# Optimization experiments

Measured on AMD Instinct MI355X. Metric: run time of the kernel, lower is better.

Reference implementation:

```python
import jax, jax.numpy as jnp
import numpy as np

NUM_LAYERS = 6
DIM = 512
VOCAB = 50257
HEADS = 8
EXPERTS = 8
TOPK = 2
LN_EPS = 1e-5


def setup_inputs() -> dict:
    key = jax.random.key(0)
    ks = jax.random.split(key, 9)
    d, L, E = DIM, NUM_LAYERS, EXPERTS
    return {
        'input_ids': jax.random.randint(ks[0], (2, 1024), 0, VOCAB),
        'embed': jax.random.normal(ks[1], (VOCAB, d), dtype=jnp.float32) * 0.02,
        'qkv_w': jax.random.normal(ks[2], (L, 3 * d, d), dtype=jnp.float32) * 0.02,
        'out_w': jax.random.normal(ks[3], (L, d, d), dtype=jnp.float32) * 0.02,
        'router_w': jax.random.normal(ks[4], (L, E, d), dtype=jnp.float32) * 0.02,
        'router_b': jnp.zeros((L, E), dtype=jnp.float32),
        'w1': jax.random.normal(ks[5], (L, E, 2 * d, d), dtype=jnp.float32) * 0.02,
        'b1': jnp.zeros((L, E, 2 * d), dtype=jnp.float32),
        'w2': jax.random.normal(ks[6], (L, E, d, 2 * d), dtype=jnp.float32) * 0.02,
        'b2': jnp.zeros((L, E, d), dtype=jnp.float32),
        'ln_g': jnp.ones((L, d), dtype=jnp.float32),
        'ln_b': jnp.zeros((L, d), dtype=jnp.float32),
        'head_w': jax.random.normal(ks[7], (VOCAB, d), dtype=jnp.float32) * 0.02,
    }


def _bit_weight(w):
    # BitNet 1.58b training-mode effective weight (STE forward value):
    # scale = mean|w| per output row; w_eff = round(w/scale).clip(-1,1) * scale
    scale = jnp.clip(jnp.mean(jnp.abs(w), axis=-1, keepdims=True), 1e-5, None)
    wq = jnp.clip(jnp.round(w / scale), -1.0, 1.0)
    w_ste = jax.lax.stop_gradient(wq - w) + w
    return w_ste * scale


def _layer_norm(x, g, b):
    mu = jnp.mean(x, axis=-1, keepdims=True)
    var = jnp.mean(jnp.square(x - mu), axis=-1, keepdims=True)
    return (x - mu) * jax.lax.rsqrt(var + LN_EPS) * g + b


def _attention(x, qkv_w, out_w):
    B, Lq, D = x.shape
    hd = D // HEADS
    qkv = (x @ qkv_w.T).reshape(B, Lq, 3, HEADS, hd).transpose(2, 0, 3, 1, 4)
    q, k, v = qkv[0], qkv[1], qkv[2]  # [B,H,L,hd]
    attn = jax.nn.softmax(jnp.einsum('bhqd,bhkd->bhqk', q, k) * hd ** -0.5, axis=-1)
    o = jnp.einsum('bhqk,bhkd->bhqd', attn, v).transpose(0, 2, 1, 3).reshape(B, Lq, D)
    return o @ out_w.T


def _moe(x, rw, rb, w1, b1, w2, b2, g, beta):
    B, Lq, D = x.shape
    N = B * Lq
    xf = x.reshape(N, D)
    probs = jax.nn.softmax(xf @ rw.T + rb, axis=-1)  # [N,E]
    vals, idx = jax.lax.top_k(probs, TOPK)
    vals = vals / (jnp.sum(vals, axis=-1, keepdims=True) + 1e-8)
    # combine weights: [N,E] (top-k indices are distinct, so sum == scatter)
    cw = jnp.sum(jax.nn.one_hot(idx, EXPERTS, dtype=xf.dtype) * vals[..., None], axis=1)
    we1 = _bit_weight(w1)  # [E,2D,D]
    we2 = _bit_weight(w2)  # [E,D,2D]
    h = jax.nn.gelu(jnp.einsum('nd,efd->enf', xf, we1) + b1[:, None, :], approximate=False)
    y = jnp.einsum('enf,edf->end', h, we2) + b2[:, None, :]  # [E,N,D]
    out = jnp.einsum('ne,end->nd', cw, y)
    return _layer_norm(out + xf, g, beta).reshape(B, Lq, D)


def reference(input_ids, embed, qkv_w, out_w, router_w, router_b, w1, b1, w2, b2, ln_g, ln_b, head_w):
    x = embed[input_ids]  # [B,L,D]
    for l in range(NUM_LAYERS):
        x = x + _attention(x, qkv_w[l], out_w[l])
        x = _moe(x, router_w[l], router_b[l], w1[l], b1[l], w2[l], b2[l], ln_g[l], ln_b[l])
    return x @ head_w.T  # logits [B,L,V]
```

## Files before the change

kernel.cpp:

```cpp
#include <hip/hip_runtime.h>
#include <math.h>
#include <stdint.h>

#define NLAYER 6
#define DIMD 512
#define HEADS 8
#define HD 64
#define EXPERTS 8
#define SEQ 1024
#define NTOK 2048
#define FF 1024
#define VOCABN 50257
#define HROWS 50304

typedef __bf16 bf16;
typedef __bf16 bf16x8 __attribute__((ext_vector_type(8)));
typedef __bf16 bf16x4 __attribute__((ext_vector_type(4)));
typedef float f32x4 __attribute__((ext_vector_type(4)));

__device__ __forceinline__ void gl_lds16(const void* g, void* l) {
  __builtin_amdgcn_global_load_lds(
      (const __attribute__((address_space(1))) void*)(uintptr_t)g,
      (__attribute__((address_space(3))) void*)(uintptr_t)l, 16, 0, 0);
}

#define LDSW(row, kg) (((row) * 32) + ((((kg) ^ (((row) >> 1) & 3))) << 3))

template <int BNT>
__global__ __launch_bounds__(256) void k_mfma_gemm(
    const bf16* __restrict__ A0, const bf16* __restrict__ A1,
    const bf16* __restrict__ B0, const bf16* __restrict__ B1,
    float* __restrict__ Cf, bf16* __restrict__ Cb0, bf16* __restrict__ Cb1,
    bf16* __restrict__ Cb2, bf16* __restrict__ E0, bf16* __restrict__ E1,
    bf16* __restrict__ E2, int M, int N, int K,
    long sA, long sB, long sCf, long sCb,
    const float* __restrict__ colScale, int csStride,
    const float* __restrict__ bias, int biasStride,
    const float* __restrict__ residual, int act, int mode,
    const int* __restrict__ mLimit, const int* __restrict__ aperm,
    int outmode) {
  constexpr int NI = BNT / 32;
  __shared__ __align__(16) bf16 As[128 * 32];
  __shared__ __align__(16) bf16 Bs[BNT * 32];
  int tid = threadIdx.x;
  int z = blockIdx.z;
  int nwg = gridDim.x * gridDim.y;
  int flat = blockIdx.y * gridDim.x + blockIdx.x;
  int qq = nwg >> 3, rr = nwg & 7;
  int xcd = flat & 7, ii = flat >> 3;
  int swz = (xcd < rr ? xcd * (qq + 1) : rr * (qq + 1) + (xcd - rr) * qq) + ii;
  int m0 = (swz % gridDim.x) * 128, n0 = (swz / gridDim.x) * BNT;
  if (mLimit && m0 >= mLimit[z]) return;
  int w = tid >> 6, lane = tid & 63;
  int wm = (w >> 1) * 64, wn = (w & 1) * (16 * NI);
  int r15 = lane & 15, kg = lane >> 4;

  int pa[3] = {0, 0, 0}, pb[3] = {0, 0, 0};
  int np = 1;
  if (mode == 3) {
    np = 2; pa[1] = 1;
  } else if (mode == 5) {
    np = 3;
    pa[1] = 0; pb[1] = 1; pa[2] = 1; pb[2] = 0;
  }

  f32x4 acc[4][NI] = {};
  int srow = tid >> 2;
  int scol = (((tid & 3) ^ ((tid >> 3) & 3))) << 3;
  long arow0, arow1;
  if (aperm) {
    arow0 = aperm[z * 2048 + m0 + srow];
    arow1 = aperm[z * 2048 + m0 + 64 + srow];
  } else {
    arow0 = m0 + srow;
    arow1 = m0 + 64 + srow;
  }
  const bf16* PA[2] = {A0, A1};
  const bf16* PB[2] = {B0, B1};
  bf16* la0 = &As[tid * 8];
  bf16* la1 = &As[64 * 32 + tid * 8];
  bf16* lb0 = &Bs[tid * 8];

  for (int p = 0; p < np; ++p) {
    const bf16* Az = PA[pa[p]] + (long)z * sA;
    const bf16* Bz = PB[pb[p]] + (long)z * sB;
    const bf16* ga0 = Az + arow0 * K + scol;
    const bf16* ga1 = Az + arow1 * K + scol;
    const bf16* gb0 = Bz + (long)(n0 + srow) * K + scol;
    const bf16* gb1 = (BNT == 128) ? Bz + (long)(n0 + 64 + srow) * K + scol
                                   : nullptr;
    for (int k0 = 0; k0 < K; k0 += 32) {
      gl_lds16(ga0, la0);
      gl_lds16(ga1, la1);
      gl_lds16(gb0, lb0);
      if constexpr (BNT == 128) gl_lds16(gb1, &Bs[64 * 32 + tid * 8]);
      ga0 += 32; ga1 += 32; gb0 += 32;
      if constexpr (BNT == 128) gb1 += 32;
      __syncthreads();
      bf16x8 af[4], bfr[NI];
#pragma unroll
      for (int mi = 0; mi < 4; ++mi) {
        int rowA = wm + mi * 16 + r15;
        af[mi] = *(const bf16x8*)&As[LDSW(rowA, kg)];
      }
#pragma unroll
      for (int ni = 0; ni < NI; ++ni) {
        int rowB = wn + ni * 16 + r15;
        bfr[ni] = *(const bf16x8*)&Bs[LDSW(rowB, kg)];
      }
#pragma unroll
      for (int mi = 0; mi < 4; ++mi)
#pragma unroll
        for (int ni = 0; ni < NI; ++ni)
          acc[mi][ni] = __builtin_amdgcn_mfma_f32_16x16x32_bf16(
              af[mi], bfr[ni], acc[mi][ni], 0, 0, 0);
      __syncthreads();
    }
  }

#pragma unroll
  for (int mi = 0; mi < 4; ++mi) {
    int rbase = m0 + wm + mi * 16 + kg * 4;
#pragma unroll
    for (int ni = 0; ni < NI; ++ni) {
      int col = n0 + wn + ni * 16 + r15;
      if (col >= N) continue;
      float scl = colScale ? colScale[z * csStride + col] : 1.f;
      float bv = bias ? bias[z * biasStride + col] : 0.f;
#pragma unroll
      for (int reg = 0; reg < 4; ++reg) {
        int row = rbase + reg;
        float v = acc[mi][ni][reg] * scl + bv;
        if (act) v = 0.5f * v * (1.f + erff(v * 0.70710678118654752f));
        if (residual) v += residual[(long)row * N + col];
        if (outmode == 2) {
          int b = row >> 10, qt = row & 1023;
          if (n0 < 512) {
            float qv = v * 0.125f;
            int h = col >> 6, d = col & 63;
            long dst = ((long)(b * 8 + h)) * ((long)SEQ * HD) +
                       (long)qt * HD + d;
            bf16 h0 = (bf16)qv;
            Cb0[dst] = h0;
            Cb1[dst] = (bf16)(qv - (float)h0);
          } else if (n0 < 1024) {
            int c2 = col - 512;
            int h = c2 >> 6, d = c2 & 63;
            long dst = ((long)(b * 8 + h)) * ((long)SEQ * HD) +
                       (long)qt * HD + d;
            bf16 h0 = (bf16)v;
            Cb2[dst] = h0;
            E0[dst] = (bf16)(v - (float)h0);
          } else {
            int c2 = col - 1024;
            int h = c2 >> 6, d = c2 & 63;
            long dst = ((long)(b * 8 + h)) * ((long)HD * SEQ) +
                       (long)d * SEQ + qt;
            bf16 h0 = (bf16)v;
            E1[dst] = h0;
            E2[dst] = (bf16)(v - (float)h0);
          }
          continue;
        }
        if (Cf) Cf[z * sCf + (long)row * N + col] = v;
        if (Cb0) {
          long cib = z * sCb + (long)row * N + col;
          bf16 h0 = (bf16)v;
          Cb0[cib] = h0;
          if (Cb1) {
            float r = v - (float)h0;
            Cb1[cib] = (bf16)r;
          }
        }
      }
    }
  }
}

__global__ __launch_bounds__(256) void k_fattn(
    const bf16* __restrict__ q0b, const bf16* __restrict__ q1b,
    const bf16* __restrict__ k0b, const bf16* __restrict__ k1b,
    const bf16* __restrict__ vt0, const bf16* __restrict__ vt1,
    bf16* __restrict__ at0, bf16* __restrict__ at1) {
  __shared__ __align__(16) bf16 Ks[2][128 * 64];
  __shared__ __align__(16) bf16 Vs[2][64 * 128];
  __shared__ __align__(16) bf16 Ps[2][64 * 128];
  int tid = threadIdx.x;
  int bh = blockIdx.y;
  int q0 = blockIdx.x * 64;
  int w = tid >> 6, lane = tid & 63;
  int r15 = lane & 15, kg = lane >> 4;
  const long bhQK = (long)bh * SEQ * HD;
  const long bhV = (long)bh * HD * SEQ;

  bf16x8 qa0[2], qa1[2];
  {
    long qoff = bhQK + (long)(q0 + w * 16 + r15) * HD;
#pragma unroll
    for (int ks = 0; ks < 2; ++ks) {
      qa0[ks] = *(const bf16x8*)&q0b[qoff + ks * 32 + kg * 8];
      qa1[ks] = *(const bf16x8*)&q1b[qoff + ks * 32 + kg * 8];
    }
  }

  auto stageK = [&](int kt) {
#pragma unroll
    for (int i = 0; i < 4; ++i) {
      int L = tid + i * 256;
      int row = L >> 3, pc = L & 7;
      int gc = pc ^ (row & 7);
      long gsrc = bhQK + (long)(kt * 128 + row) * HD + gc * 8;
      gl_lds16(k0b + gsrc, &Ks[0][L * 8]);
      gl_lds16(k1b + gsrc, &Ks[1][L * 8]);
    }
  };
  auto stageV = [&](int kt) {
#pragma unroll
    for (int i = 0; i < 4; ++i) {
      int L = tid + i * 256;
      int row = L >> 4, pc = L & 15;
      int gc = pc ^ (row & 15);
      long gsrc = bhV + (long)row * SEQ + kt * 128 + gc * 8;
      gl_lds16(vt0 + gsrc, &Vs[0][L * 8]);
      gl_lds16(vt1 + gsrc, &Vs[1][L * 8]);
    }
  };
  auto computeS = [&](f32x4* sf) {
#pragma unroll
    for (int kc = 0; kc < 8; ++kc) {
      f32x4 a = {};
      int rowB = kc * 16 + r15;
#pragma unroll
      for (int ks = 0; ks < 2; ++ks) {
        int pc = (ks * 4 + kg) ^ (rowB & 7);
        bf16x8 b0 = *(const bf16x8*)&Ks[0][rowB * 64 + pc * 8];
        bf16x8 b1 = *(const bf16x8*)&Ks[1][rowB * 64 + pc * 8];
        a = __builtin_amdgcn_mfma_f32_16x16x32_bf16(qa0[ks], b0, a, 0, 0, 0);
        a = __builtin_amdgcn_mfma_f32_16x16x32_bf16(qa0[ks], b1, a, 0, 0, 0);
        a = __builtin_amdgcn_mfma_f32_16x16x32_bf16(qa1[ks], b0, a, 0, 0, 0);
      }
      sf[kc] = a;
    }
  };

  float m[4], l[4];
#pragma unroll
  for (int r = 0; r < 4; ++r) { m[r] = -1e30f; l[r] = 0.f; }

  for (int kt = 0; kt < SEQ / 128; ++kt) {
    stageK(kt);
    __syncthreads();
    f32x4 sf[8];
    computeS(sf);
#pragma unroll
    for (int r = 0; r < 4; ++r) {
      float tm = sf[0][r];
#pragma unroll
      for (int kc = 1; kc < 8; ++kc) tm = fmaxf(tm, sf[kc][r]);
      tm = fmaxf(tm, __shfl_xor(tm, 1));
      tm = fmaxf(tm, __shfl_xor(tm, 2));
      tm = fmaxf(tm, __shfl_xor(tm, 4));
      tm = fmaxf(tm, __shfl_xor(tm, 8));
      float mn = fmaxf(m[r], tm);
      float corr = __expf(m[r] - mn);
      float s = 0.f;
#pragma unroll
      for (int kc = 0; kc < 8; ++kc) s += __expf(sf[kc][r] - mn);
      s += __shfl_xor(s, 1);
      s += __shfl_xor(s, 2);
      s += __shfl_xor(s, 4);
      s += __shfl_xor(s, 8);
      l[r] = l[r] * corr + s;
      m[r] = mn;
    }
    __syncthreads();
  }

  float invl[4];
#pragma unroll
  for (int r = 0; r < 4; ++r) invl[r] = 1.f / l[r];

  f32x4 oacc[4] = {};
  for (int kt = 0; kt < SEQ / 128; ++kt) {
    stageK(kt);
    stageV(kt);
    __syncthreads();
    f32x4 sf[8];
    computeS(sf);
#pragma unroll
    for (int kc = 0; kc < 8; ++kc) {
#pragma unroll
      for (int r = 0; r < 4; ++r) {
        float p = __expf(sf[kc][r] - m[r]) * invl[r];
        bf16 h0 = (bf16)p;
        bf16 h1 = (bf16)(p - (float)h0);
        int qrow = w * 16 + kg * 4 + r;
        int kcol = kc * 16 + r15;
        int pc = (kcol >> 3) ^ (qrow & 15);
        int addr = qrow * 128 + pc * 8 + (kcol & 7);
        Ps[0][addr] = h0;
        Ps[1][addr] = h1;
      }
    }
    __syncthreads();
    bf16x8 pa0[4], pa1[4];
    int rowP = w * 16 + r15;
#pragma unroll
    for (int ks = 0; ks < 4; ++ks) {
      int pc = (ks * 4 + kg) ^ (rowP & 15);
      pa0[ks] = *(const bf16x8*)&Ps[0][rowP * 128 + pc * 8];
      pa1[ks] = *(const bf16x8*)&Ps[1][rowP * 128 + pc * 8];
    }
#pragma unroll
    for (int dg = 0; dg < 4; ++dg) {
      int rowV = dg * 16 + r15;
#pragma unroll
      for (int ks = 0; ks < 4; ++ks) {
        int pc = (ks * 4 + kg) ^ (rowV & 15);
        bf16x8 v0 = *(const bf16x8*)&Vs[0][rowV * 128 + pc * 8];
        bf16x8 v1 = *(const bf16x8*)&Vs[1][rowV * 128 + pc * 8];
        oacc[dg] = __builtin_amdgcn_mfma_f32_16x16x32_bf16(pa0[ks], v0,
                                                           oacc[dg], 0, 0, 0);
        oacc[dg] = __builtin_amdgcn_mfma_f32_16x16x32_bf16(pa0[ks], v1,
                                                           oacc[dg], 0, 0, 0);
        oacc[dg] = __builtin_amdgcn_mfma_f32_16x16x32_bf16(pa1[ks], v0,
                                                           oacc[dg], 0, 0, 0);
      }
    }
    __syncthreads();
  }

  int b = bh >> 3, h = bh & 7;
#pragma unroll
  for (int dg = 0; dg < 4; ++dg) {
#pragma unroll
    for (int r = 0; r < 4; ++r) {
      int qrow = q0 + w * 16 + kg * 4 + r;
      int d = dg * 16 + r15;
      long dst = ((long)(b * SEQ + qrow)) * DIMD + h * HD + d;
      float v = oacc[dg][r];
      bf16 h0 = (bf16)v;
      at0[dst] = h0;
      at1[dst] = (bf16)(v - (float)h0);
    }
  }
}

__global__ __launch_bounds__(256) void k_hgemm(const bf16* __restrict__ A,
                                               const bf16* __restrict__ Bt,
                                               float* __restrict__ C,
                                               int M, int N, int K) {
  __shared__ __align__(16) bf16 As[128 * 64];
  __shared__ __align__(16) bf16 Bs[128 * 64];
  int tid = threadIdx.x;
  int nwg = gridDim.x * gridDim.y;
  int flat = blockIdx.y * gridDim.x + blockIdx.x;
  int qq = nwg >> 3, rr = nwg & 7;
  int xcd = flat & 7, ii = flat >> 3;
  int swz = (xcd < rr ? xcd * (qq + 1) : rr * (qq + 1) + (xcd - rr) * qq) + ii;
  int m0 = (swz % gridDim.x) * 128, n0 = (swz / gridDim.x) * 128;
  int w = tid >> 6, lane = tid & 63;
  int wm = (w >> 1) * 64, wn = (w & 1) * 64;
  int r15 = lane & 15, kg = lane >> 4;
  int srow = tid >> 3;
  int scol = (((tid & 7) ^ ((tid >> 3) & 7))) << 3;
  const bf16* ga = A + (long)(m0 + srow) * K + scol;
  const bf16* gb = Bt + (long)(n0 + srow) * K + scol;
  f32x4 acc[4][4] = {};
  for (int k0 = 0; k0 < K; k0 += 64) {
#pragma unroll
    for (int i = 0; i < 4; ++i) {
      gl_lds16(ga + (long)i * 32 * K + k0, &As[i * 2048 + tid * 8]);
      gl_lds16(gb + (long)i * 32 * K + k0, &Bs[i * 2048 + tid * 8]);
    }
    __syncthreads();
#pragma unroll
    for (int kk = 0; kk < 2; ++kk) {
      bf16x8 af[4], bf_[4];
#pragma unroll
      for (int mi = 0; mi < 4; ++mi) {
        int rowA = wm + mi * 16 + r15;
        af[mi] = *(const bf16x8*)
            &As[rowA * 64 + ((((kk * 4 + kg) ^ (rowA & 7))) << 3)];
      }
#pragma unroll
      for (int ni = 0; ni < 4; ++ni) {
        int rowB = wn + ni * 16 + r15;
        bf_[ni] = *(const bf16x8*)
            &Bs[rowB * 64 + ((((kk * 4 + kg) ^ (rowB & 7))) << 3)];
      }
#pragma unroll
      for (int mi = 0; mi < 4; ++mi)
#pragma unroll
        for (int ni = 0; ni < 4; ++ni)
          acc[mi][ni] = __builtin_amdgcn_mfma_f32_16x16x32_bf16(
              af[mi], bf_[ni], acc[mi][ni], 0, 0, 0);
    }
    __syncthreads();
  }
#pragma unroll
  for (int mi = 0; mi < 4; ++mi) {
    int rbase = m0 + wm + mi * 16 + kg * 4;
#pragma unroll
    for (int ni = 0; ni < 4; ++ni) {
      int col = n0 + wn + ni * 16 + r15;
      if (col >= N) continue;
#pragma unroll
      for (int reg = 0; reg < 4; ++reg)
        C[(long)(rbase + reg) * N + col] = acc[mi][ni][reg];
    }
  }
}

__global__ __launch_bounds__(256) void k_embed(const int* __restrict__ ids,
                                               const float* __restrict__ E,
                                               float* __restrict__ xf,
                                               bf16* __restrict__ x0,
                                               bf16* __restrict__ x1) {
  int i = blockIdx.x * 256 + threadIdx.x;
  if (i >= NTOK * DIMD) return;
  int n = i >> 9, d = i & 511;
  float v = E[(long)ids[n] * DIMD + d];
  xf[i] = v;
  bf16 b0 = (bf16)v;
  x0[i] = b0;
  x1[i] = (bf16)(v - (float)b0);
}

__global__ __launch_bounds__(256) void k_prepw(const float* __restrict__ qw,
                                               const float* __restrict__ ow,
                                               bf16* __restrict__ qw0,
                                               bf16* __restrict__ qw1,
                                               bf16* __restrict__ ow0,
                                               bf16* __restrict__ ow1) {
  const long n8q = (long)3 * DIMD * DIMD / 8;
  long i = (long)blockIdx.x * 256 + threadIdx.x;
  const float* s;
  bf16 *d0, *d1;
  long j;
  if (i < n8q) {
    s = qw; d0 = qw0; d1 = qw1; j = i;
  } else {
    s = ow; d0 = ow0; d1 = ow1; j = i - n8q;
  }
  const float4* s4 = (const float4*)s;
  float4 a = s4[2 * j], b = s4[2 * j + 1];
  float vv[8] = {a.x, a.y, a.z, a.w, b.x, b.y, b.z, b.w};
  bf16x8 o0, o1;
#pragma unroll
  for (int k = 0; k < 8; ++k) {
    float v = vv[k];
    bf16 h0 = (bf16)v;
    o0[k] = h0;
    o1[k] = (bf16)(v - (float)h0);
  }
  ((bf16x8*)d0)[j] = o0;
  ((bf16x8*)d1)[j] = o1;
}

__global__ __launch_bounds__(256) void k_headconv(const float* __restrict__ s,
                                                  bf16* __restrict__ d) {
  long i = (long)blockIdx.x * 256 + threadIdx.x;
  long n8 = (long)HROWS * DIMD / 8;
  if (i >= n8) return;
  long row = i / (DIMD / 8);
  bf16x8 o;
  if (row < VOCABN) {
    const float4* s4 = (const float4*)s;
    float4 a = s4[2 * i], b = s4[2 * i + 1];
    o[0] = (bf16)a.x; o[1] = (bf16)a.y; o[2] = (bf16)a.z; o[3] = (bf16)a.w;
    o[4] = (bf16)b.x; o[5] = (bf16)b.y; o[6] = (bf16)b.z; o[7] = (bf16)b.w;
  } else {
    o = (bf16x8)(bf16)0.f;
  }
  ((bf16x8*)d)[i] = o;
}

__global__ __launch_bounds__(64) void k_router(const float* __restrict__ x,
                                               const float* __restrict__ rw,
                                               const float* __restrict__ rb,
                                               int* __restrict__ top2,
                                               float* __restrict__ v2) {
  int n = blockIdx.x;
  int t = threadIdx.x;
  int e = t >> 3, part = t & 7;
  __shared__ float red[64];
  const float* xr = x + (long)n * DIMD;
  const float* wr = rw + (long)e * DIMD;
  float d = 0.f;
  int c0 = part * 64;
#pragma unroll
  for (int c = 0; c < 64; c += 4) {
    float4 xv = *(const float4*)(xr + c0 + c);
    float4 wv = *(const float4*)(wr + c0 + c);
    d += xv.x * wv.x + xv.y * wv.y + xv.z * wv.z + xv.w * wv.w;
  }
  red[t] = d;
  __syncthreads();
  if (t < 8) {
    float logit = rb[t];
    for (int pp = 0; pp < 8; ++pp) logit += red[t * 8 + pp];
    red[t] = logit;
  }
  __syncthreads();
  if (t == 0) {
    float p2[8];
    float m = -1e30f;
    for (int i = 0; i < 8; ++i) m = fmaxf(m, red[i]);
    float s = 0.f;
    for (int i = 0; i < 8; ++i) { p2[i] = expf(red[i] - m); s += p2[i]; }
    for (int i = 0; i < 8; ++i) p2[i] /= s;
    int i1 = 0;
    for (int i = 1; i < 8; ++i) if (p2[i] > p2[i1]) i1 = i;
    int i2 = (i1 == 0) ? 1 : 0;
    for (int i = 0; i < 8; ++i) {
      if (i == i1 || i == i2) continue;
      if (p2[i] > p2[i2]) i2 = i;
    }
    float sum = p2[i1] + p2[i2] + 1e-8f;
    top2[2 * n] = i1;
    top2[2 * n + 1] = i2;
    v2[2 * n] = p2[i1] / sum;
    v2[2 * n + 1] = p2[i2] / sum;
  }
}

__global__ __launch_bounds__(256) void k_expcnt(const int* __restrict__ top2,
                                                int* __restrict__ perm,
                                                int* __restrict__ tokpos,
                                                int* __restrict__ cnt,
                                                bf16* __restrict__ zx0,
                                                bf16* __restrict__ zx1) {
  int e = blockIdx.x, t = threadIdx.x;
  if (e == 0) {
    for (int c = t; c < DIMD; c += 256) {
      zx0[c] = (bf16)0.f;
      zx1[c] = (bf16)0.f;
    }
  }
  __shared__ int sc[256];
  int fl[8];
  int f = 0;
#pragma unroll
  for (int j = 0; j < 8; ++j) {
    int n = t * 8 + j;
    int m = (top2[2 * n] == e || top2[2 * n + 1] == e) ? 1 : 0;
    fl[j] = m;
    f += m;
  }
  sc[t] = f;
  __syncthreads();
  for (int o = 1; o < 256; o <<= 1) {
    int v = (t >= o) ? sc[t - o] : 0;
    __syncthreads();
    sc[t] += v;
    __syncthreads();
  }
  int pos = sc[t] - f;
#pragma unroll
  for (int j = 0; j < 8; ++j) {
    if (fl[j]) {
      int n = t * 8 + j;
      perm[e * 2048 + pos] = n;
      int jj = (top2[2 * n] == e) ? 0 : 1;
      tokpos[2 * n + jj] = e * 2048 + pos;
      ++pos;
    }
  }
  int total = sc[255];
  int cpad = (total + 127) & ~127;
  for (int i = total + t; i < cpad; i += 256) perm[e * 2048 + i] = 2048;
  if (t == 0) cnt[e] = total;
}

__global__ __launch_bounds__(256) void k_bitw2(const float* __restrict__ w1l,
                                               const float* __restrict__ w2l,
                                               bf16* __restrict__ we1q,
                                               float* __restrict__ s1,
                                               bf16* __restrict__ we2q,
                                               float* __restrict__ s2) {
  int blk = blockIdx.x;
  int t = threadIdx.x;
  const float* wr;
  bf16* outr;
  float* sOut;
  int cols;
  if (blk < EXPERTS * FF) {
    cols = DIMD;
    wr = w1l + (long)blk * cols;
    outr = we1q + (long)blk * cols;
    sOut = s1 + blk;
  } else {
    int row = blk - EXPERTS * FF;
    cols = FF;
    wr = w2l + (long)row * cols;
    outr = we2q + (long)row * cols;
    sOut = s2 + row;
  }
  float acc = 0.f;
  for (int c = t; c < cols; c += 256) acc += fabsf(wr[c]);
  __shared__ float red[256];
  red[t] = acc;
  __syncthreads();
  for (int off = 128; off; off >>= 1) {
    if (t < off) red[t] += red[t + off];
    __syncthreads();
  }
  float scale = fmaxf(red[0] / (float)cols, 1e-5f);
  if (t == 0) *sOut = scale;
  for (int c = t; c < cols; c += 256) {
    float qv = rintf(wr[c] / scale);
    qv = fmaxf(-1.f, fminf(1.f, qv));
    outr[c] = (bf16)qv;
  }
}

__global__ __launch_bounds__(128) void k_lncomb(
    const float* __restrict__ yg, const int* __restrict__ tokpos,
    const float* __restrict__ v2, const float* __restrict__ xBf,
    const float* __restrict__ g, const float* __restrict__ b,
    float* __restrict__ xof, bf16* __restrict__ x0, bf16* __restrict__ x1) {
  int n = blockIdx.x;
  int t = threadIdx.x;
  __shared__ float red[128];
  long tp0 = tokpos[2 * n], tp1 = tokpos[2 * n + 1];
  float w0 = v2[2 * n], w1 = v2[2 * n + 1];
  const float* y0 = yg + tp0 * DIMD;
  const float* y1 = yg + tp1 * DIMD;
  float u[4];
  float s = 0.f;
#pragma unroll
  for (int i = 0; i < 4; ++i) {
    int d = t + i * 128;
    float v = xBf[(long)n * DIMD + d] + w0 * y0[d] + w1 * y1[d];
    u[i] = v;
    s += v;
  }
  red[t] = s;
  __syncthreads();
  for (int off = 64; off; off >>= 1) {
    if (t < off) red[t] += red[t + off];
    __syncthreads();
  }
  float mu = red[0] / (float)DIMD;
  __syncthreads();
  float var = 0.f;
#pragma unroll
  for (int i = 0; i < 4; ++i) {
    float d = u[i] - mu;
    var += d * d;
  }
  red[t] = var;
  __syncthreads();
  for (int off = 64; off; off >>= 1) {
    if (t < off) red[t] += red[t + off];
    __syncthreads();
  }
  float inv = 1.f / sqrtf(red[0] / (float)DIMD + 1e-5f);
#pragma unroll
  for (int i = 0; i < 4; ++i) {
    int c = t + i * 128;
    float v = (u[i] - mu) * inv * g[c] + b[c];
    long oi = (long)n * DIMD + c;
    xof[oi] = v;
    bf16 b0 = (bf16)v;
    x0[oi] = b0;
    x1[oi] = (bf16)(v - (float)b0);
  }
}

extern "C" void kernel_launch(void* const* d_in, const int* in_sizes, int n_in,
                              void* d_out, int out_size, void* d_ws, size_t ws_size,
                              hipStream_t stream) {
  const int* ids = (const int*)d_in[0];
  const float* embed = (const float*)d_in[1];
  const float* qkv_w = (const float*)d_in[2];
  const float* out_w = (const float*)d_in[3];
  const float* router_w = (const float*)d_in[4];
  const float* router_b = (const float*)d_in[5];
  const float* w1 = (const float*)d_in[6];
  const float* b1 = (const float*)d_in[7];
  const float* w2 = (const float*)d_in[8];
  const float* b2 = (const float*)d_in[9];
  const float* ln_g = (const float*)d_in[10];
  const float* ln_b = (const float*)d_in[11];
  const float* head_w = (const float*)d_in[12];
  float* out = (float*)d_out;

  char* base = (char*)d_ws;
  size_t off = 0;
  auto alloc = [&](size_t bytes) -> void* {
    void* p = base + off;
    off += (bytes + 255) & ~(size_t)255;
    return p;
  };
  const size_t ND = (size_t)NTOK * DIMD;
  float* xAf = (float*)alloc(ND * 4);
  float* xBf = (float*)alloc(ND * 4);
  int* top2 = (int*)alloc((size_t)NTOK * 2 * 4);
  float* v2 = (float*)alloc((size_t)NTOK * 2 * 4);
  int* perm = (int*)alloc((size_t)EXPERTS * 2048 * 4);
  int* tokpos = (int*)alloc((size_t)NTOK * 2 * 4);
  int* cntb = (int*)alloc(64);
  bf16* xA0 = (bf16*)alloc(ND * 2);
  bf16* xA1 = (bf16*)alloc(ND * 2);
  bf16* xB0 = (bf16*)alloc((ND + DIMD) * 2);
  bf16* xB1 = (bf16*)alloc((ND + DIMD) * 2);
  bf16* at0 = (bf16*)alloc(ND * 2);
  bf16* at1 = (bf16*)alloc(ND * 2);
  bf16* qw0 = (bf16*)alloc((size_t)3 * DIMD * DIMD * 2);
  bf16* qw1 = (bf16*)alloc((size_t)3 * DIMD * DIMD * 2);
  bf16* ow0 = (bf16*)alloc((size_t)DIMD * DIMD * 2);
  bf16* ow1 = (bf16*)alloc((size_t)DIMD * DIMD * 2);
  bf16* q0b = (bf16*)alloc((size_t)16 * SEQ * HD * 2);
  bf16* q1b = (bf16*)alloc((size_t)16 * SEQ * HD * 2);
  bf16* k0b = (bf16*)alloc((size_t)16 * SEQ * HD * 2);
  bf16* k1b = (bf16*)alloc((size_t)16 * SEQ * HD * 2);
  bf16* vt0b = (bf16*)alloc((size_t)16 * HD * SEQ * 2);
  bf16* vt1b = (bf16*)alloc((size_t)16 * HD * SEQ * 2);

  size_t Ustart = off;
  bf16* we1q = (bf16*)alloc((size_t)EXPERTS * FF * DIMD * 2);
  float* s1 = (float*)alloc((size_t)EXPERTS * FF * 4);
  bf16* we2q = (bf16*)alloc((size_t)EXPERTS * DIMD * FF * 2);
  float* s2 = (float*)alloc((size_t)EXPERTS * DIMD * 4);
  bf16* h0g = (bf16*)alloc((size_t)EXPERTS * 2048 * FF * 2);
  bf16* h1g = (bf16*)alloc((size_t)EXPERTS * 2048 * FF * 2);
  float* yg = (float*)alloc((size_t)EXPERTS * 2048 * DIMD * 4);
  size_t endB = off;
  size_t endC = Ustart + (size_t)HROWS * DIMD * 2;
  bf16* hw0 = (bf16*)(base + Ustart);
  off = endB > endC ? endB : endC;
  if (ws_size < off) return;

  k_embed<<<(NTOK * DIMD + 255) / 256, 256, 0, stream>>>(ids, embed, xAf, xA0,
                                                         xA1);

  for (int l = 0; l < NLAYER; ++l) {
    const float* qw = qkv_w + (long)l * 3 * DIMD * DIMD;
    const float* ow = out_w + (long)l * DIMD * DIMD;
    k_prepw<<<512, 256, 0, stream>>>(qw, ow, qw0, qw1, ow0, ow1);
    k_mfma_gemm<128><<<dim3(NTOK / 128, (3 * DIMD) / 128, 1), 256, 0,
                       stream>>>(
        xA0, xA1, qw0, qw1, nullptr, q0b, q1b, k0b, k1b, vt0b, vt1b,
        NTOK, 3 * DIMD, DIMD, 0, 0, 0, 0,
        nullptr, 0, nullptr, 0, nullptr, 0, 5, nullptr, nullptr, 2);
    k_fattn<<<dim3(SEQ / 64, 16), 256, 0, stream>>>(q0b, q1b, k0b, k1b,
                                                    vt0b, vt1b, at0, at1);
    k_mfma_gemm<128><<<dim3(NTOK / 128, DIMD / 128, 1), 256, 0, stream>>>(
        at0, at1, ow0, ow1, xBf, xB0, xB1, nullptr, nullptr, nullptr,
        nullptr, NTOK, DIMD, DIMD, 0, 0, 0, 0,
        nullptr, 0, nullptr, 0, xAf, 0, 5, nullptr, nullptr, 0);
    k_router<<<NTOK, 64, 0, stream>>>(xBf, router_w + (long)l * EXPERTS * DIMD,
                                      router_b + l * EXPERTS, top2, v2);
    k_expcnt<<<EXPERTS, 256, 0, stream>>>(top2, perm, tokpos, cntb,
                                          xB0 + ND, xB1 + ND);
    k_bitw2<<<EXPERTS * FF + EXPERTS * DIMD, 256, 0, stream>>>(
        w1 + (long)l * EXPERTS * FF * DIMD, w2 + (long)l * EXPERTS * DIMD * FF,
        we1q, s1, we2q, s2);
    k_mfma_gemm<128><<<dim3(NTOK / 128, FF / 128, EXPERTS), 256, 0, stream>>>(
        xB0, xB1, we1q, nullptr, nullptr, h0g, h1g, nullptr, nullptr, nullptr,
        nullptr, NTOK, FF, DIMD, 0, (long)FF * DIMD, 0, (long)2048 * FF,
        s1, FF, b1 + (long)l * EXPERTS * FF, FF, nullptr, 1, 3, cntb, perm, 0);
    k_mfma_gemm<128><<<dim3(NTOK / 128, DIMD / 128, EXPERTS), 256, 0,
                       stream>>>(
        h0g, h1g, we2q, nullptr, yg, nullptr, nullptr, nullptr, nullptr,
        nullptr, nullptr, NTOK, DIMD, FF, (long)2048 * FF, (long)DIMD * FF,
        (long)2048 * DIMD, 0, s2, DIMD, b2 + (long)l * EXPERTS * DIMD, DIMD,
        nullptr, 0, 3, cntb, nullptr, 0);
    k_lncomb<<<NTOK, 128, 0, stream>>>(yg, tokpos, v2, xBf, ln_g + l * DIMD,
                                       ln_b + l * DIMD, xAf, xA0, xA1);
  }
  long nh8 = (long)HROWS * DIMD / 8;
  k_headconv<<<(int)((nh8 + 255) / 256), 256, 0, stream>>>(head_w, hw0);
  k_hgemm<<<dim3(NTOK / 128, HROWS / 128, 1), 256, 0, stream>>>(
      xA0, hw0, out, NTOK, VOCABN, DIMD);
}
```

Baseline: 2.368 ms.

## Use single-pass online-softmax attention and batch weight prep across layers

The attention kernel now runs one pass over K/V with online softmax rescaling of the output accumulator, instead of a max/sum pass followed by a second pass that recomputes QK^T. This removes one full QK^T recomputation and one K staging per tile, and drops a barrier. Separately, weight conversion and BitNet quantization for all layers are launched once up front into per-layer buffers, replacing per-layer launches. This needs much more workspace and no longer reuses the shared region for the quantized expert weights.

```diff
diff --git a/kernel.cpp b/kernel.cpp
--- a/kernel.cpp
+++ b/kernel.cpp
@@ -246,9 +246,11 @@
   float m[4], l[4];
 #pragma unroll
   for (int r = 0; r < 4; ++r) { m[r] = -1e30f; l[r] = 0.f; }
+  f32x4 oacc[4] = {};
 
   for (int kt = 0; kt < SEQ / 128; ++kt) {
     stageK(kt);
+    stageV(kt);
     __syncthreads();
     f32x4 sf[8];
     computeS(sf);
@@ -265,33 +267,25 @@
       float corr = __expf(m[r] - mn);
       float s = 0.f;
 #pragma unroll
-      for (int kc = 0; kc < 8; ++kc) s += __expf(sf[kc][r] - mn);
+      for (int kc = 0; kc < 8; ++kc) {
+        float p = __expf(sf[kc][r] - mn);
+        sf[kc][r] = p;
+        s += p;
+      }
       s += __shfl_xor(s, 1);
       s += __shfl_xor(s, 2);
       s += __shfl_xor(s, 4);
       s += __shfl_xor(s, 8);
       l[r] = l[r] * corr + s;
       m[r] = mn;
-    }
-    __syncthreads();
-  }
-
-  float invl[4];
-#pragma unroll
-  for (int r = 0; r < 4; ++r) invl[r] = 1.f / l[r];
-
-  f32x4 oacc[4] = {};
-  for (int kt = 0; kt < SEQ / 128; ++kt) {
-    stageK(kt);
-    stageV(kt);
-    __syncthreads();
-    f32x4 sf[8];
-    computeS(sf);
+#pragma unroll
+      for (int dg = 0; dg < 4; ++dg) oacc[dg][r] *= corr;
+    }
 #pragma unroll
     for (int kc = 0; kc < 8; ++kc) {
 #pragma unroll
       for (int r = 0; r < 4; ++r) {
-        float p = __expf(sf[kc][r] - m[r]) * invl[r];
+        float p = sf[kc][r];
         bf16 h0 = (bf16)p;
         bf16 h1 = (bf16)(p - (float)h0);
         int qrow = w * 16 + kg * 4 + r;
@@ -302,7 +296,6 @@
         Ps[1][addr] = h1;
       }
     }
-    __syncthreads();
     bf16x8 pa0[4], pa1[4];
     int rowP = w * 16 + r15;
 #pragma unroll
@@ -330,6 +323,10 @@
     __syncthreads();
   }
 
+  float invl[4];
+#pragma unroll
+  for (int r = 0; r < 4; ++r) invl[r] = 1.f / l[r];
+
   int b = bh >> 3, h = bh & 7;
 #pragma unroll
   for (int dg = 0; dg < 4; ++dg) {
@@ -338,7 +335,7 @@
       int qrow = q0 + w * 16 + kg * 4 + r;
       int d = dg * 16 + r15;
       long dst = ((long)(b * SEQ + qrow)) * DIMD + h * HD + d;
-      float v = oacc[dg][r];
+      float v = oacc[dg][r] * invl[r];
       bf16 h0 = (bf16)v;
       at0[dst] = h0;
       at1[dst] = (bf16)(v - (float)h0);
@@ -427,21 +424,28 @@
   x1[i] = (bf16)(v - (float)b0);
 }
 
-__global__ __launch_bounds__(256) void k_prepw(const float* __restrict__ qw,
-                                               const float* __restrict__ ow,
-                                               bf16* __restrict__ qw0,
-                                               bf16* __restrict__ qw1,
-                                               bf16* __restrict__ ow0,
-                                               bf16* __restrict__ ow1) {
+__global__ __launch_bounds__(256) void k_prepw(const float* __restrict__ qkv_w,
+                                               const float* __restrict__ out_w,
+                                               bf16* __restrict__ qw0a,
+                                               bf16* __restrict__ qw1a,
+                                               bf16* __restrict__ ow0a,
+                                               bf16* __restrict__ ow1a) {
+  int l = blockIdx.y;
   const long n8q = (long)3 * DIMD * DIMD / 8;
   long i = (long)blockIdx.x * 256 + threadIdx.x;
   const float* s;
   bf16 *d0, *d1;
   long j;
   if (i < n8q) {
-    s = qw; d0 = qw0; d1 = qw1; j = i;
+    s = qkv_w + (long)l * 3 * DIMD * DIMD;
+    d0 = qw0a + (long)l * 3 * DIMD * DIMD;
+    d1 = qw1a + (long)l * 3 * DIMD * DIMD;
+    j = i;
   } else {
-    s = ow; d0 = ow0; d1 = ow1; j = i - n8q;
+    s = out_w + (long)l * DIMD * DIMD;
+    d0 = ow0a + (long)l * DIMD * DIMD;
+    d1 = ow1a + (long)l * DIMD * DIMD;
+    j = i - n8q;
   }
   const float4* s4 = (const float4*)s;
   float4 a = s4[2 * j], b = s4[2 * j + 1];
@@ -573,12 +577,13 @@
   if (t == 0) cnt[e] = total;
 }
 
-__global__ __launch_bounds__(256) void k_bitw2(const float* __restrict__ w1l,
-                                               const float* __restrict__ w2l,
-                                               bf16* __restrict__ we1q,
-                                               float* __restrict__ s1,
-                                               bf16* __restrict__ we2q,
-                                               float* __restrict__ s2) {
+__global__ __launch_bounds__(256) void k_bitw2(const float* __restrict__ w1,
+                                               const float* __restrict__ w2,
+                                               bf16* __restrict__ we1qa,
+                                               float* __restrict__ s1a,
+                                               bf16* __restrict__ we2qa,
+                                               float* __restrict__ s2a) {
+  int l = blockIdx.y;
   int blk = blockIdx.x;
   int t = threadIdx.x;
   const float* wr;
@@ -587,15 +592,15 @@
   int cols;
   if (blk < EXPERTS * FF) {
     cols = DIMD;
-    wr = w1l + (long)blk * cols;
-    outr = we1q + (long)blk * cols;
-    sOut = s1 + blk;
+    wr = w1 + (long)l * EXPERTS * FF * DIMD + (long)blk * cols;
+    outr = we1qa + (long)l * EXPERTS * FF * DIMD + (long)blk * cols;
+    sOut = s1a + (long)l * EXPERTS * FF + blk;
   } else {
     int row = blk - EXPERTS * FF;
     cols = FF;
-    wr = w2l + (long)row * cols;
-    outr = we2q + (long)row * cols;
-    sOut = s2 + row;
+    wr = w2 + (long)l * EXPERTS * DIMD * FF + (long)row * cols;
+    outr = we2qa + (long)l * EXPERTS * DIMD * FF + (long)row * cols;
+    sOut = s2a + (long)l * EXPERTS * DIMD + row;
   }
   float acc = 0.f;
   for (int c = t; c < cols; c += 256) acc += fabsf(wr[c]);
@@ -708,22 +713,22 @@
   bf16* xB1 = (bf16*)alloc((ND + DIMD) * 2);
   bf16* at0 = (bf16*)alloc(ND * 2);
   bf16* at1 = (bf16*)alloc(ND * 2);
-  bf16* qw0 = (bf16*)alloc((size_t)3 * DIMD * DIMD * 2);
-  bf16* qw1 = (bf16*)alloc((size_t)3 * DIMD * DIMD * 2);
-  bf16* ow0 = (bf16*)alloc((size_t)DIMD * DIMD * 2);
-  bf16* ow1 = (bf16*)alloc((size_t)DIMD * DIMD * 2);
   bf16* q0b = (bf16*)alloc((size_t)16 * SEQ * HD * 2);
   bf16* q1b = (bf16*)alloc((size_t)16 * SEQ * HD * 2);
   bf16* k0b = (bf16*)alloc((size_t)16 * SEQ * HD * 2);
   bf16* k1b = (bf16*)alloc((size_t)16 * SEQ * HD * 2);
   bf16* vt0b = (bf16*)alloc((size_t)16 * HD * SEQ * 2);
   bf16* vt1b = (bf16*)alloc((size_t)16 * HD * SEQ * 2);
+  bf16* qw0a = (bf16*)alloc((size_t)NLAYER * 3 * DIMD * DIMD * 2);
+  bf16* qw1a = (bf16*)alloc((size_t)NLAYER * 3 * DIMD * DIMD * 2);
+  bf16* ow0a = (bf16*)alloc((size_t)NLAYER * DIMD * DIMD * 2);
+  bf16* ow1a = (bf16*)alloc((size_t)NLAYER * DIMD * DIMD * 2);
+  bf16* we1qa = (bf16*)alloc((size_t)NLAYER * EXPERTS * FF * DIMD * 2);
+  float* s1a = (float*)alloc((size_t)NLAYER * EXPERTS * FF * 4);
+  bf16* we2qa = (bf16*)alloc((size_t)NLAYER * EXPERTS * DIMD * FF * 2);
+  float* s2a = (float*)alloc((size_t)NLAYER * EXPERTS * DIMD * 4);
 
   size_t Ustart = off;
-  bf16* we1q = (bf16*)alloc((size_t)EXPERTS * FF * DIMD * 2);
-  float* s1 = (float*)alloc((size_t)EXPERTS * FF * 4);
-  bf16* we2q = (bf16*)alloc((size_t)EXPERTS * DIMD * FF * 2);
-  float* s2 = (float*)alloc((size_t)EXPERTS * DIMD * 4);
   bf16* h0g = (bf16*)alloc((size_t)EXPERTS * 2048 * FF * 2);
   bf16* h1g = (bf16*)alloc((size_t)EXPERTS * 2048 * FF * 2);
   float* yg = (float*)alloc((size_t)EXPERTS * 2048 * DIMD * 4);
@@ -735,11 +740,20 @@
 
   k_embed<<<(NTOK * DIMD + 255) / 256, 256, 0, stream>>>(ids, embed, xAf, xA0,
                                                          xA1);
+  k_prepw<<<dim3(512, NLAYER), 256, 0, stream>>>(qkv_w, out_w, qw0a, qw1a,
+                                                 ow0a, ow1a);
+  k_bitw2<<<dim3(EXPERTS * FF + EXPERTS * DIMD, NLAYER), 256, 0, stream>>>(
+      w1, w2, we1qa, s1a, we2qa, s2a);
 
   for (int l = 0; l < NLAYER; ++l) {
-    const float* qw = qkv_w + (long)l * 3 * DIMD * DIMD;
-    const float* ow = out_w + (long)l * DIMD * DIMD;
-    k_prepw<<<512, 256, 0, stream>>>(qw, ow, qw0, qw1, ow0, ow1);
+    bf16* qw0 = qw0a + (long)l * 3 * DIMD * DIMD;
+    bf16* qw1 = qw1a + (long)l * 3 * DIMD * DIMD;
+    bf16* ow0 = ow0a + (long)l * DIMD * DIMD;
+    bf16* ow1 = ow1a + (long)l * DIMD * DIMD;
+    bf16* we1q = we1qa + (long)l * EXPERTS * FF * DIMD;
+    bf16* we2q = we2qa + (long)l * EXPERTS * DIMD * FF;
+    float* s1 = s1a + (long)l * EXPERTS * FF;
+    float* s2 = s2a + (long)l * EXPERTS * DIMD;
     k_mfma_gemm<128><<<dim3(NTOK / 128, (3 * DIMD) / 128, 1), 256, 0,
                        stream>>>(
         xA0, xA1, qw0, qw1, nullptr, q0b, q1b, k0b, k1b, vt0b, vt1b,
@@ -755,9 +769,6 @@
                                       router_b + l * EXPERTS, top2, v2);
     k_expcnt<<<EXPERTS, 256, 0, stream>>>(top2, perm, tokpos, cntb,
                                           xB0 + ND, xB1 + ND);
-    k_bitw2<<<EXPERTS * FF + EXPERTS * DIMD, 256, 0, stream>>>(
-        w1 + (long)l * EXPERTS * FF * DIMD, w2 + (long)l * EXPERTS * DIMD * FF,
-        we1q, s1, we2q, s2);
     k_mfma_gemm<128><<<dim3(NTOK / 128, FF / 128, EXPERTS), 256, 0, stream>>>(
         xB0, xB1, we1q, nullptr, nullptr, h0g, h1g, nullptr, nullptr, nullptr,
         nullptr, NTOK, FF, DIMD, 0, (long)FF * DIMD, 0, (long)2048 * FF,
```

Result: faster. 2.309 ms (-2.5%).
